# Kernel optimization log

Hardware: AMD Instinct MI355X
Metric: run time of the kernel (lower is better)

## Reference

```python
import jax, jax.numpy as jnp
import numpy as np

HIDDEN = 1024
ATTN = 512


def setup_inputs() -> dict:
    key = jax.random.key(0)
    ks = jax.random.split(key, 7)
    B, S = 8, 2048
    inputs = jax.random.normal(ks[0], (B, S, HIDDEN), dtype=jnp.float32)
    s = 1.0 / np.sqrt(HIDDEN)
    Wq = jax.random.uniform(ks[1], (HIDDEN, ATTN), jnp.float32, -s, s)
    bq = jax.random.uniform(ks[2], (ATTN,), jnp.float32, -s, s)
    Wk = jax.random.uniform(ks[3], (HIDDEN, ATTN), jnp.float32, -s, s)
    bk = jax.random.uniform(ks[4], (ATTN,), jnp.float32, -s, s)
    Wv = jax.random.uniform(ks[5], (HIDDEN, ATTN), jnp.float32, -s, s)
    bv = jax.random.uniform(ks[6], (ATTN,), jnp.float32, -s, s)
    return {"inputs": inputs, "Wq": Wq, "bq": bq, "Wk": Wk, "bk": bk, "Wv": Wv, "bv": bv}


def reference(inputs, Wq, bq, Wk, bk, Wv, bv):
    # tanh-gated Q/K/V projections
    q = jnp.tanh(inputs @ Wq + bq)        # [B, S, A]
    k = jnp.tanh(inputs @ Wk + bk)        # [B, S, A]
    v = jnp.tanh(inputs @ Wv + bv)        # [B, S, A]
    scores = jnp.einsum('bqa,bka->bqk', q, k) / jnp.sqrt(jnp.float32(ATTN))
    probs = jax.nn.softmax(scores, axis=-1)   # [B, S, S]
    context = jnp.einsum('bqk,bka->bqa', probs, v)
    return jnp.tanh(context), probs
```

## Files before the change

kernel.cpp:

```cpp
#include <hip/hip_runtime.h>
#include <hip/hip_fp16.h>
#include <cstdint>

#define HIDDEN 1024
#define ATTN   512
#define NB     8
#define SEQ    2048
#define MROWS  (NB*SEQ)

typedef _Float16 f16x8 __attribute__((ext_vector_type(8)));
typedef _Float16 f16x4 __attribute__((ext_vector_type(4)));
typedef float    f32x4 __attribute__((ext_vector_type(4)));


__device__ __forceinline__ float tanh_fast(float x){
  float e = __expf(2.0f*x);
  return 1.0f - 2.0f/(e + 1.0f);
}

__device__ __forceinline__ void gload16(const void* g, void* l){
  __builtin_amdgcn_global_load_lds((const __attribute__((address_space(1))) void*)g,
                                   (__attribute__((address_space(3))) void*)l, 16, 0, 0);
}

__global__ __launch_bounds__(256) void k_cast_x(const float* __restrict__ x, __half* __restrict__ xh){
  size_t i = (size_t)blockIdx.x*256 + threadIdx.x;
  const float4* src = reinterpret_cast<const float4*>(x) + i*2;
  float4 a = src[0], b = src[1];
  f16x8 h;
  h[0]=(_Float16)a.x; h[1]=(_Float16)a.y; h[2]=(_Float16)a.z; h[3]=(_Float16)a.w;
  h[4]=(_Float16)b.x; h[5]=(_Float16)b.y; h[6]=(_Float16)b.z; h[7]=(_Float16)b.w;
  reinterpret_cast<f16x8*>(xh)[i] = h;
}

__global__ __launch_bounds__(256) void k_transpose_w(const float* __restrict__ Wq, const float* __restrict__ Wk,
                                                     const float* __restrict__ Wv, __half* __restrict__ whT){
  __shared__ float lds[32][33];
  int which = blockIdx.y;
  const float* W = which==0 ? Wq : (which==1 ? Wk : Wv);
  int tr = blockIdx.x >> 4;
  int tc = blockIdx.x & 15;
  int t = threadIdx.x;
  {
    int r = t >> 3, c4 = (t & 7)*4;
    float4 v = *reinterpret_cast<const float4*>(W + (size_t)(tr*32 + r)*ATTN + tc*32 + c4);
    lds[r][c4+0]=v.x; lds[r][c4+1]=v.y; lds[r][c4+2]=v.z; lds[r][c4+3]=v.w;
  }
  __syncthreads();
  {
    int n = t >> 3, k4 = (t & 7)*4;
    ushort4 u;
    u.x = __half_as_ushort(__float2half(lds[k4+0][n]));
    u.y = __half_as_ushort(__float2half(lds[k4+1][n]));
    u.z = __half_as_ushort(__float2half(lds[k4+2][n]));
    u.w = __half_as_ushort(__float2half(lds[k4+3][n]));
    *reinterpret_cast<ushort4*>(whT + (size_t)which*ATTN*HIDDEN + (size_t)(tc*32 + n)*HIDDEN + tr*32 + k4) = u;
  }
}

__global__ __launch_bounds__(256,3) void k_proj(const __half* __restrict__ xh, const __half* __restrict__ whT,
                                                const float* __restrict__ bq, const float* __restrict__ bk,
                                                const float* __restrict__ bv,
                                                __half* __restrict__ qh, __half* __restrict__ kh, __half* __restrict__ vT){
  __shared__ __align__(16) _Float16 lA[128*64];
  __shared__ __align__(16) _Float16 lB[128*64];
  int nt = blockIdx.x;
  int m0 = blockIdx.y * 128;
  int which = nt >> 2;
  int ncol0 = (nt & 3) * 128;
  int t = threadIdx.x;
  int w = t >> 6, lane = t & 63;
  int lrow = lane & 15, lk = lane >> 4;
  int wm = w >> 1, wn = w & 1;

  int rr = lane >> 3;
  int ss = (lane & 7) ^ rr;
  const __half* Abase = xh + (size_t)(m0 + w*32 + rr)*HIDDEN + ss*8;
  const __half* Bbase = whT + (size_t)which*ATTN*HIDDEN + (size_t)(ncol0 + w*32 + rr)*HIDDEN + ss*8;
  _Float16* lAw = &lA[(w*32)*64];
  _Float16* lBw = &lB[(w*32)*64];

  f32x4 acc[4][4];
  #pragma unroll
  for (int i=0;i<4;i++)
    #pragma unroll
    for (int j=0;j<4;j++) acc[i][j] = f32x4{0.f,0.f,0.f,0.f};

  for (int k0 = 0; k0 < HIDDEN; k0 += 64){
    __syncthreads();
    #pragma unroll
    for (int c=0; c<4; c++){
      gload16(Abase + (size_t)c*8*HIDDEN + k0, &lAw[c*8*64]);
      gload16(Bbase + (size_t)c*8*HIDDEN + k0, &lBw[c*8*64]);
    }
    __syncthreads();
    #pragma unroll
    for (int u=0; u<2; u++){
      f16x8 af[4], bf[4];
      #pragma unroll
      for (int fm=0; fm<4; fm++){
        int row = wm*64 + fm*16 + lrow;
        af[fm] = *(const f16x8*)&lA[row*64 + (((u*4 + lk) ^ (row & 7))*8)];
      }
      #pragma unroll
      for (int fn=0; fn<4; fn++){
        int row = wn*64 + fn*16 + lrow;
        bf[fn] = *(const f16x8*)&lB[row*64 + (((u*4 + lk) ^ (row & 7))*8)];
      }
      #pragma unroll
      for (int fm=0; fm<4; fm++)
        #pragma unroll
        for (int fn=0; fn<4; fn++)
          acc[fm][fn] = __builtin_amdgcn_mfma_f32_16x16x32_f16(af[fm], bf[fn], acc[fm][fn], 0,0,0);
    }
  }

  const float* bias = which==0 ? bq : (which==1 ? bk : bv);
  if (which < 2){
    __half* dst = which==0 ? qh : kh;
    int rt_base = (m0 >> 4) + wm*4;
    int at_base = (ncol0 >> 5) + wn*2;
    #pragma unroll
    for (int fn=0; fn<4; fn++){
      int col = ncol0 + wn*64 + fn*16 + lrow;
      float bb = bias[col];
      int at = at_base + (fn >> 1);
      int asub = (fn & 1)*16 + lrow;
      #pragma unroll
      for (int fm=0; fm<4; fm++){
        size_t tbase = (size_t)(rt_base + fm)*8192 + (size_t)at*512 + asub;
        #pragma unroll
        for (int mi=0; mi<4; mi++)
          dst[tbase + (lk*4 + mi)*32] = __float2half(tanh_fast(acc[fm][fn][mi] + bb));
      }
    }
  } else {
    __half* vb = vT + (size_t)(m0 >> 11)*ATTN*SEQ;
    int jb0 = (m0 & 2047) + wm*64;
    int at0 = (ncol0 >> 4) + wn*4;
    #pragma unroll
    for (int fn=0; fn<4; fn++){
      int col = ncol0 + wn*64 + fn*16 + lrow;
      float bb = bias[col];
      #pragma unroll
      for (int fm=0; fm<4; fm++){
        int jb = jb0 + fm*16;
        f16x4 h;
        #pragma unroll
        for (int mi=0; mi<4; mi++) h[mi] = (_Float16)tanh_fast(acc[fm][fn][mi] + bb);
        *(f16x4*)(vb + (size_t)(at0 + fn)*32768 + (size_t)(jb >> 5)*512 + lrow*32 + (jb & 16) + lk*4) = h;
      }
    }
  }
}

__global__ __launch_bounds__(512,2) void k_scoresE(const __half* __restrict__ qh, const __half* __restrict__ kh,
                                                   __half* __restrict__ p16){
  __shared__ __align__(16) _Float16 qlds[4*16*512];
  __shared__ __align__(16) _Float16 khlds[32*512];
  int bid = blockIdx.x;
  int b  = bid & 7;
  int i0 = (bid >> 3) * 64;
  int t = threadIdx.x;
  int w = t >> 6, lane = t & 63;
  int lrow = lane & 15, lk = lane >> 4;

  const __half* qsrc = qh + (size_t)((b*SEQ + i0) >> 4)*8192;
  const __half* ksrc = kh + (size_t)b*SEQ*ATTN;
  __half* pb = p16 + (size_t)b*SEQ*SEQ;

  #pragma unroll
  for (int r=0; r<8; r++){
    int chunk = r*8 + w;
    gload16(qsrc + (size_t)chunk*512 + lane*8, &qlds[chunk*512]);
  }

  const float scale = 0.044194173824159216f;
  for (int ko = 0; ko < 4; ko++){
    f32x4 acc[4][4];
    #pragma unroll
    for (int i=0;i<4;i++)
      #pragma unroll
      for (int j=0;j<4;j++) acc[i][j] = f32x4{0.f,0.f,0.f,0.f};

    for (int it = 0; it < 16; it++){
      __syncthreads();
      #pragma unroll
      for (int j=0; j<4; j++){
        int c = w*4 + j;
        gload16(ksrc + (size_t)(ko*32 + c)*8192 + it*512 + lane*8, &khlds[c*512]);
      }
      __syncthreads();
      f16x8 kf[4], qf[4];
      #pragma unroll
      for (int j=0;j<4;j++) kf[j] = *(const f16x8*)&khlds[(w*4+j)*512 + lrow*32 + lk*8];
      #pragma unroll
      for (int j=0;j<4;j++) qf[j] = *(const f16x8*)&qlds[(j*16 + it)*512 + lrow*32 + lk*8];
      #pragma unroll
      for (int fn=0; fn<4; fn++)
        #pragma unroll
        for (int qi=0; qi<4; qi++)
          acc[qi][fn] = __builtin_amdgcn_mfma_f32_16x16x32_f16(kf[fn], qf[qi], acc[qi][fn], 0,0,0);
    }

    #pragma unroll
    for (int qi=0; qi<4; qi++){
      size_t tq = (size_t)((i0 >> 4) + qi)*32768;
      #pragma unroll
      for (int fn=0; fn<4; fn++){
        f16x4 h;
        #pragma unroll
        for (int mi=0; mi<4; mi++) h[mi] = (_Float16)__expf(acc[qi][fn][mi]*scale);
        *(f16x4*)&pb[tq + (size_t)(ko*16 + w*2 + (fn>>1))*512 + lrow*32 + (fn&1)*16 + lk*4] = h;
      }
    }
  }
}

__global__ __launch_bounds__(1024,4) void k_scores(const __half* __restrict__ qh, const __half* __restrict__ kh,
                                                   float* __restrict__ probs){
  __shared__ float red[16][32];
  int bid = blockIdx.x;
  int b  = bid & 7;
  int i0 = (bid >> 3) * 32;
  int t = threadIdx.x;
  int w = t >> 6, lane = t & 63;
  int lrow = lane & 15, lk = lane >> 4;
  int loff = lrow*32 + lk*8;

  const __half* kbase = kh + (size_t)((b*SEQ + w*128) >> 4)*8192 + loff;
  const __half* qbase = qh + (size_t)((b*SEQ + i0) >> 4)*8192 + loff;

  f32x4 acc[2][8];
  #pragma unroll
  for (int i=0;i<2;i++)
    #pragma unroll
    for (int j=0;j<8;j++) acc[i][j] = f32x4{0.f,0.f,0.f,0.f};

  for (int it = 0; it < 16; it++){
    f16x8 aq0 = *(const f16x8*)(qbase + it*512);
    f16x8 aq1 = *(const f16x8*)(qbase + 8192 + it*512);
    #pragma unroll
    for (int fn=0; fn<8; fn++){
      f16x8 kf = *(const f16x8*)(kbase + (size_t)fn*8192 + it*512);
      acc[0][fn] = __builtin_amdgcn_mfma_f32_16x16x32_f16(kf, aq0, acc[0][fn], 0,0,0);
      acc[1][fn] = __builtin_amdgcn_mfma_f32_16x16x32_f16(kf, aq1, acc[1][fn], 0,0,0);
    }
  }

  const float scale = 0.044194173824159216f;
  float sm[2];
  #pragma unroll
  for (int nf=0;nf<2;nf++){
    float s = 0.f;
    #pragma unroll
    for (int fn=0;fn<8;fn++)
      #pragma unroll
      for (int mi=0;mi<4;mi++){
        float e = __expf(acc[nf][fn][mi] * scale);
        acc[nf][fn][mi] = e;
        s += e;
      }
    s += __shfl_xor(s, 16);
    s += __shfl_xor(s, 32);
    sm[nf] = s;
  }
  if (lane < 16){ red[w][lane] = sm[0]; red[w][16 + lane] = sm[1]; }
  __syncthreads();
  float inv[2];
  #pragma unroll
  for (int nf=0;nf<2;nf++){
    float tot = 0.f;
    #pragma unroll
    for (int ww=0; ww<16; ww++) tot += red[ww][nf*16 + lrow];
    inv[nf] = 1.0f / tot;
  }
  #pragma unroll
  for (int nf=0;nf<2;nf++){
    f32x4 iv = {inv[nf], inv[nf], inv[nf], inv[nf]};
    #pragma unroll
    for (int fn=0;fn<8;fn++){
      f32x4 v = acc[nf][fn] * iv;
      size_t rowoff = (size_t)(i0 + nf*16 + lrow)*SEQ + w*128 + lk*4;
      *(f32x4*)(probs + (size_t)b*SEQ*SEQ + rowoff + fn*16) = v;
    }
  }
}

__global__ __launch_bounds__(512,4) void k_pv_p16(const __half* __restrict__ p16, const __half* __restrict__ vT,
                                                  float* __restrict__ probs, float* __restrict__ out0){
  __shared__ float partial[8][64];
  __shared__ float rsum[64];
  int bid = blockIdx.x;
  int b  = bid & 7;
  int i0 = (bid >> 3) * 64;
  int t = threadIdx.x;
  int w = t >> 6, lane = t & 63;
  int lrow = lane & 15, lk = lane >> 4;
  int loff = lrow*32 + lk*8;

  const __half* pbase = p16 + (size_t)b*SEQ*SEQ + (size_t)(i0 >> 4)*32768 + loff;
  const __half* vbase = vT + (size_t)b*ATTN*SEQ + (size_t)(w*4)*32768 + loff;

  f32x4 acc[4][4];
  #pragma unroll
  for (int i=0;i<4;i++)
    #pragma unroll
    for (int j=0;j<4;j++) acc[i][j] = f32x4{0.f,0.f,0.f,0.f};
  float esum[4] = {0.f,0.f,0.f,0.f};

  for (int kt = 0; kt < 64; kt++){
    f16x8 pa[4];
    #pragma unroll
    for (int nf=0; nf<4; nf++)
      pa[nf] = *(const f16x8*)(pbase + (size_t)nf*32768 + kt*512);
    if ((kt >> 3) == w){
      #pragma unroll
      for (int nf=0; nf<4; nf++){
        float s = 0.f;
        #pragma unroll
        for (int j=0; j<8; j++) s += (float)pa[nf][j];
        esum[nf] += s;
      }
    }
    #pragma unroll
    for (int cf=0; cf<4; cf++){
      f16x8 bv8 = *(const f16x8*)(vbase + (size_t)cf*32768 + kt*512);
      #pragma unroll
      for (int nf=0; nf<4; nf++)
        acc[nf][cf] = __builtin_amdgcn_mfma_f32_16x16x32_f16(pa[nf], bv8, acc[nf][cf], 0,0,0);
    }
  }

  #pragma unroll
  for (int nf=0; nf<4; nf++){
    esum[nf] += __shfl_xor(esum[nf], 16);
    esum[nf] += __shfl_xor(esum[nf], 32);
  }
  if (lane < 16){
    #pragma unroll
    for (int nf=0; nf<4; nf++) partial[w][nf*16 + lane] = esum[nf];
  }
  __syncthreads();
  if (t < 64){
    float s = 0.f;
    #pragma unroll
    for (int ww=0; ww<8; ww++) s += partial[ww][t];
    rsum[t] = s;
  }
  __syncthreads();

  float* dst = out0 + ((size_t)b*SEQ + i0)*ATTN + w*64;
  #pragma unroll
  for (int nf=0; nf<4; nf++)
    #pragma unroll
    for (int mi=0; mi<4; mi++){
      float iv = 1.0f / rsum[nf*16 + lk*4 + mi];
      #pragma unroll
      for (int cf=0; cf<4; cf++)
        __builtin_nontemporal_store(tanh_fast(acc[nf][cf][mi]*iv),
                                    dst + (size_t)(nf*16 + lk*4 + mi)*ATTN + cf*16 + lrow);
    }

  float* prow = probs + ((size_t)b*SEQ + i0 + lrow)*SEQ + lk*8;
  #pragma unroll
  for (int nf=0; nf<4; nf++){
    float iv = 1.0f / rsum[nf*16 + lrow];
    #pragma unroll
    for (int k2=0; k2<8; k2++){
      int kt = w*8 + k2;
      f16x8 pa = *(const f16x8*)(pbase + (size_t)nf*32768 + kt*512);
      f32x4 lo = {(float)pa[0]*iv, (float)pa[1]*iv, (float)pa[2]*iv, (float)pa[3]*iv};
      f32x4 hi = {(float)pa[4]*iv, (float)pa[5]*iv, (float)pa[6]*iv, (float)pa[7]*iv};
      float* pr = prow + (size_t)nf*16*SEQ + kt*32;
      __builtin_nontemporal_store(lo, (f32x4*)(pr));
      __builtin_nontemporal_store(hi, (f32x4*)(pr + 4));
    }
  }
}

__global__ __launch_bounds__(512,4) void k_pv(const float* __restrict__ probs, const __half* __restrict__ vT,
                                              float* __restrict__ out0){
  int bid = blockIdx.x;
  int b  = bid & 7;
  int i0 = (bid >> 3) * 32;
  int t = threadIdx.x;
  int w = t >> 6, lane = t & 63;
  int lrow = lane & 15, lk = lane >> 4;
  int loff = lrow*32 + lk*8;

  const float* pbase = probs + ((size_t)b*SEQ + i0 + lrow)*SEQ + lk*8;
  const __half* vbase = vT + (size_t)b*ATTN*SEQ + (size_t)(w*4)*32768 + loff;

  f32x4 acc[2][4];
  #pragma unroll
  for (int i=0;i<2;i++)
    #pragma unroll
    for (int j=0;j<4;j++) acc[i][j] = f32x4{0.f,0.f,0.f,0.f};

  for (int kt = 0; kt < 64; kt++){
    int k0 = kt*32;
    f16x8 af[2];
    #pragma unroll
    for (int nf=0; nf<2; nf++){
      const float* pr = pbase + (size_t)nf*16*SEQ + k0;
      float4 a = *(const float4*)(pr);
      float4 c = *(const float4*)(pr + 4);
      f16x8 h;
      h[0]=(_Float16)a.x; h[1]=(_Float16)a.y; h[2]=(_Float16)a.z; h[3]=(_Float16)a.w;
      h[4]=(_Float16)c.x; h[5]=(_Float16)c.y; h[6]=(_Float16)c.z; h[7]=(_Float16)c.w;
      af[nf] = h;
    }
    #pragma unroll
    for (int cf=0; cf<4; cf++){
      f16x8 bv8 = *(const f16x8*)(vbase + (size_t)cf*32768 + kt*512);
      acc[0][cf] = __builtin_amdgcn_mfma_f32_16x16x32_f16(af[0], bv8, acc[0][cf], 0,0,0);
      acc[1][cf] = __builtin_amdgcn_mfma_f32_16x16x32_f16(af[1], bv8, acc[1][cf], 0,0,0);
    }
  }

  float* dst = out0 + ((size_t)b*SEQ + i0)*ATTN + w*64;
  #pragma unroll
  for (int nf=0; nf<2; nf++)
    #pragma unroll
    for (int cf=0; cf<4; cf++)
      #pragma unroll
      for (int mi=0; mi<4; mi++)
        dst[(size_t)(nf*16 + lk*4 + mi)*ATTN + cf*16 + lrow] = tanh_fast(acc[nf][cf][mi]);
}

extern "C" void kernel_launch(void* const* d_in, const int* in_sizes, int n_in,
                              void* d_out, int out_size, void* d_ws, size_t ws_size,
                              hipStream_t stream){
  const float* x  = (const float*)d_in[0];
  const float* Wq = (const float*)d_in[1];
  const float* bq = (const float*)d_in[2];
  const float* Wk = (const float*)d_in[3];
  const float* bk = (const float*)d_in[4];
  const float* Wv = (const float*)d_in[5];
  const float* bv = (const float*)d_in[6];

  float* out0 = (float*)d_out;
  float* out1 = out0 + (size_t)NB*SEQ*ATTN;

  const size_t SZ = 16777216;
  char* ws = (char*)d_ws;

  if (ws_size >= 5*SZ){
    __half* vT  = (__half*)ws;
    __half* p16 = (__half*)(ws + SZ);
    __half* xh  = (__half*)out1;
    __half* whT = (__half*)((char*)out1 + 2*SZ);
    __half* qh  = (__half*)((char*)out1 + 2*SZ + 3145728);
    __half* kh  = (__half*)((char*)out1 + 3*SZ + 3145728);
    k_cast_x     <<<8192,        256, 0, stream>>>(x, xh);
    k_transpose_w<<<dim3(512,3), 256, 0, stream>>>(Wq, Wk, Wv, whT);
    k_proj       <<<dim3(12,128),256, 0, stream>>>(xh, whT, bq, bk, bv, qh, kh, vT);
    k_scoresE    <<<256,         512, 0, stream>>>(qh, kh, p16);
    k_pv_p16     <<<256,         512, 0, stream>>>(p16, vT, out1, out0);
  } else if (ws_size >= 3*SZ){
    __half* vT = (__half*)ws;
    __half* qh = (__half*)(ws + SZ);
    __half* kh = (__half*)(ws + 2*SZ);
    __half* xh  = (__half*)out1;
    __half* whT = (__half*)((char*)out1 + 2*SZ);
    k_cast_x     <<<8192,        256, 0, stream>>>(x, xh);
    k_transpose_w<<<dim3(512,3), 256, 0, stream>>>(Wq, Wk, Wv, whT);
    k_proj       <<<dim3(12,128),256, 0, stream>>>(xh, whT, bq, bk, bv, qh, kh, vT);
    k_scores     <<<512,        1024, 0, stream>>>(qh, kh, out1);
    k_pv         <<<512,         512, 0, stream>>>(out1, vT, out0);
  } else {
    __half* vT = (__half*)ws;
    __half* qh = (__half*)out0;
    __half* kh = (__half*)out0 + (size_t)MROWS*ATTN;
    __half* xh  = (__half*)out1;
    __half* whT = (__half*)((char*)out1 + 2*SZ);
    k_cast_x     <<<8192,        256, 0, stream>>>(x, xh);
    k_transpose_w<<<dim3(512,3), 256, 0, stream>>>(Wq, Wk, Wv, whT);
    k_proj       <<<dim3(12,128),256, 0, stream>>>(xh, whT, bq, bk, bv, qh, kh, vT);
    k_scores     <<<512,        1024, 0, stream>>>(qh, kh, out1);
    k_pv         <<<512,         512, 0, stream>>>(out1, vT, out0);
  }
}
```

Before: 282.2 us.

## Split probs expansion and row sums into separate kernel; double K tile per sync

Moves the fp16-to-fp32 probability expansion and the softmax row-sum computation out of the P·V kernel into a new k_expand kernel. That kernel stages a 16-row tile in LDS, reduces the row sums, writes them to workspace and streams out the normalized fp32 probs. The P·V kernel now only does MFMA work plus a normalized tanh epilogue, reading the precomputed sums. The scores kernel also loads two K tiles per barrier pair, halving its syncs at the cost of double the K staging LDS. The risks are an extra launch, rereading p16, and the new path now needing slightly more workspace than before.

```diff
diff --git a/kernel.cpp b/kernel.cpp
--- a/kernel.cpp
+++ b/kernel.cpp
@@ -157,7 +157,7 @@
 __global__ __launch_bounds__(512,2) void k_scoresE(const __half* __restrict__ qh, const __half* __restrict__ kh,
                                                    __half* __restrict__ p16){
   __shared__ __align__(16) _Float16 qlds[4*16*512];
-  __shared__ __align__(16) _Float16 khlds[32*512];
+  __shared__ __align__(16) _Float16 khlds[64*512];
   int bid = blockIdx.x;
   int b  = bid & 7;
   int i0 = (bid >> 3) * 64;
@@ -183,24 +183,28 @@
       #pragma unroll
       for (int j=0;j<4;j++) acc[i][j] = f32x4{0.f,0.f,0.f,0.f};
 
-    for (int it = 0; it < 16; it++){
+    for (int it = 0; it < 16; it += 2){
       __syncthreads();
       #pragma unroll
       for (int j=0; j<4; j++){
         int c = w*4 + j;
-        gload16(ksrc + (size_t)(ko*32 + c)*8192 + it*512 + lane*8, &khlds[c*512]);
+        gload16(ksrc + (size_t)(ko*32 + c)*8192 + it*512 + lane*8,       &khlds[c*512]);
+        gload16(ksrc + (size_t)(ko*32 + c)*8192 + (it+1)*512 + lane*8,   &khlds[(32 + c)*512]);
       }
       __syncthreads();
-      f16x8 kf[4], qf[4];
-      #pragma unroll
-      for (int j=0;j<4;j++) kf[j] = *(const f16x8*)&khlds[(w*4+j)*512 + lrow*32 + lk*8];
-      #pragma unroll
-      for (int j=0;j<4;j++) qf[j] = *(const f16x8*)&qlds[(j*16 + it)*512 + lrow*32 + lk*8];
-      #pragma unroll
-      for (int fn=0; fn<4; fn++)
-        #pragma unroll
-        for (int qi=0; qi<4; qi++)
-          acc[qi][fn] = __builtin_amdgcn_mfma_f32_16x16x32_f16(kf[fn], qf[qi], acc[qi][fn], 0,0,0);
+      #pragma unroll
+      for (int half=0; half<2; half++){
+        f16x8 kf[4], qf[4];
+        #pragma unroll
+        for (int j=0;j<4;j++) kf[j] = *(const f16x8*)&khlds[(half*32 + w*4+j)*512 + lrow*32 + lk*8];
+        #pragma unroll
+        for (int j=0;j<4;j++) qf[j] = *(const f16x8*)&qlds[(j*16 + it + half)*512 + lrow*32 + lk*8];
+        #pragma unroll
+        for (int fn=0; fn<4; fn++)
+          #pragma unroll
+          for (int qi=0; qi<4; qi++)
+            acc[qi][fn] = __builtin_amdgcn_mfma_f32_16x16x32_f16(kf[fn], qf[qi], acc[qi][fn], 0,0,0);
+      }
     }
 
     #pragma unroll
@@ -213,6 +217,63 @@
         for (int mi=0; mi<4; mi++) h[mi] = (_Float16)__expf(acc[qi][fn][mi]*scale);
         *(f16x4*)&pb[tq + (size_t)(ko*16 + w*2 + (fn>>1))*512 + lrow*32 + (fn&1)*16 + lk*4] = h;
       }
+    }
+  }
+}
+
+__global__ __launch_bounds__(256,4) void k_expand(const __half* __restrict__ p16,
+                                                  float* __restrict__ probs, float* __restrict__ rsumg){
+  __shared__ __align__(16) _Float16 lds[16*2048];
+  __shared__ float partial[16][16];
+  __shared__ float rs[16];
+  int bid = blockIdx.x;
+  int b  = bid & 7;
+  int tq = bid >> 3;
+  int t = threadIdx.x;
+  int w = t >> 6, lane = t & 63;
+
+  const __half* src = p16 + (size_t)b*SEQ*SEQ + (size_t)tq*32768;
+  #pragma unroll
+  for (int i=0; i<16; i++){
+    int chunk = i*4 + w;
+    gload16(src + (size_t)chunk*512 + lane*8, &lds[chunk*512]);
+  }
+  __syncthreads();
+
+  {
+    int r = t & 15, seg = t >> 4;
+    float s = 0.f;
+    #pragma unroll
+    for (int c8=0; c8<16; c8++){
+      int c = seg*128 + c8*8;
+      f16x8 v = *(const f16x8*)&lds[(c >> 5)*512 + r*32 + (c & 31)];
+      #pragma unroll
+      for (int j=0;j<8;j++) s += (float)v[j];
+    }
+    partial[seg][r] = s;
+  }
+  __syncthreads();
+  if (t < 16){
+    float s = 0.f;
+    #pragma unroll
+    for (int seg=0; seg<16; seg++) s += partial[seg][t];
+    rs[t] = s;
+    rsumg[(size_t)b*SEQ + tq*16 + t] = s;
+  }
+  __syncthreads();
+
+  float* pbase = probs + ((size_t)b*SEQ + tq*16)*SEQ;
+  #pragma unroll
+  for (int rr=0; rr<4; rr++){
+    int r = rr*4 + w;
+    float iv = 1.0f / rs[r];
+    float* prow = pbase + (size_t)r*SEQ;
+    #pragma unroll
+    for (int ki=0; ki<8; ki++){
+      int c = ki*256 + lane*4;
+      f16x4 v = *(const f16x4*)&lds[(c >> 5)*512 + r*32 + (c & 31)];
+      f32x4 o = {(float)v[0]*iv, (float)v[1]*iv, (float)v[2]*iv, (float)v[3]*iv};
+      __builtin_nontemporal_store(o, (f32x4*)(prow + c));
     }
   }
 }
@@ -288,9 +349,7 @@
 }
 
 __global__ __launch_bounds__(512,4) void k_pv_p16(const __half* __restrict__ p16, const __half* __restrict__ vT,
-                                                  float* __restrict__ probs, float* __restrict__ out0){
-  __shared__ float partial[8][64];
-  __shared__ float rsum[64];
+                                                  const float* __restrict__ rsumg, float* __restrict__ out0){
   int bid = blockIdx.x;
   int b  = bid & 7;
   int i0 = (bid >> 3) * 64;
@@ -307,22 +366,12 @@
   for (int i=0;i<4;i++)
     #pragma unroll
     for (int j=0;j<4;j++) acc[i][j] = f32x4{0.f,0.f,0.f,0.f};
-  float esum[4] = {0.f,0.f,0.f,0.f};
 
   for (int kt = 0; kt < 64; kt++){
     f16x8 pa[4];
     #pragma unroll
     for (int nf=0; nf<4; nf++)
       pa[nf] = *(const f16x8*)(pbase + (size_t)nf*32768 + kt*512);
-    if ((kt >> 3) == w){
-      #pragma unroll
-      for (int nf=0; nf<4; nf++){
-        float s = 0.f;
-        #pragma unroll
-        for (int j=0; j<8; j++) s += (float)pa[nf][j];
-        esum[nf] += s;
-      }
-    }
     #pragma unroll
     for (int cf=0; cf<4; cf++){
       f16x8 bv8 = *(const f16x8*)(vbase + (size_t)cf*32768 + kt*512);
@@ -332,49 +381,17 @@
     }
   }
 
+  float* dst = out0 + ((size_t)b*SEQ + i0)*ATTN + w*64;
   #pragma unroll
   for (int nf=0; nf<4; nf++){
-    esum[nf] += __shfl_xor(esum[nf], 16);
-    esum[nf] += __shfl_xor(esum[nf], 32);
-  }
-  if (lane < 16){
-    #pragma unroll
-    for (int nf=0; nf<4; nf++) partial[w][nf*16 + lane] = esum[nf];
-  }
-  __syncthreads();
-  if (t < 64){
-    float s = 0.f;
-    #pragma unroll
-    for (int ww=0; ww<8; ww++) s += partial[ww][t];
-    rsum[t] = s;
-  }
-  __syncthreads();
-
-  float* dst = out0 + ((size_t)b*SEQ + i0)*ATTN + w*64;
-  #pragma unroll
-  for (int nf=0; nf<4; nf++)
+    f32x4 rs4 = *(const f32x4*)&rsumg[(size_t)b*SEQ + i0 + nf*16 + lk*4];
     #pragma unroll
     for (int mi=0; mi<4; mi++){
-      float iv = 1.0f / rsum[nf*16 + lk*4 + mi];
+      float iv = 1.0f / rs4[mi];
       #pragma unroll
       for (int cf=0; cf<4; cf++)
         __builtin_nontemporal_store(tanh_fast(acc[nf][cf][mi]*iv),
                                     dst + (size_t)(nf*16 + lk*4 + mi)*ATTN + cf*16 + lrow);
-    }
-
-  float* prow = probs + ((size_t)b*SEQ + i0 + lrow)*SEQ + lk*8;
-  #pragma unroll
-  for (int nf=0; nf<4; nf++){
-    float iv = 1.0f / rsum[nf*16 + lrow];
-    #pragma unroll
-    for (int k2=0; k2<8; k2++){
-      int kt = w*8 + k2;
-      f16x8 pa = *(const f16x8*)(pbase + (size_t)nf*32768 + kt*512);
-      f32x4 lo = {(float)pa[0]*iv, (float)pa[1]*iv, (float)pa[2]*iv, (float)pa[3]*iv};
-      f32x4 hi = {(float)pa[4]*iv, (float)pa[5]*iv, (float)pa[6]*iv, (float)pa[7]*iv};
-      float* pr = prow + (size_t)nf*16*SEQ + kt*32;
-      __builtin_nontemporal_store(lo, (f32x4*)(pr));
-      __builtin_nontemporal_store(hi, (f32x4*)(pr + 4));
     }
   }
 }
@@ -446,9 +463,10 @@
   const size_t SZ = 16777216;
   char* ws = (char*)d_ws;
 
-  if (ws_size >= 5*SZ){
-    __half* vT  = (__half*)ws;
-    __half* p16 = (__half*)(ws + SZ);
+  if (ws_size >= 5*SZ + 65536){
+    __half* vT    = (__half*)ws;
+    __half* p16   = (__half*)(ws + SZ);
+    float*  rsumg = (float*)(ws + 5*SZ);
     __half* xh  = (__half*)out1;
     __half* whT = (__half*)((char*)out1 + 2*SZ);
     __half* qh  = (__half*)((char*)out1 + 2*SZ + 3145728);
@@ -457,7 +475,8 @@
     k_transpose_w<<<dim3(512,3), 256, 0, stream>>>(Wq, Wk, Wv, whT);
     k_proj       <<<dim3(12,128),256, 0, stream>>>(xh, whT, bq, bk, bv, qh, kh, vT);
     k_scoresE    <<<256,         512, 0, stream>>>(qh, kh, p16);
-    k_pv_p16     <<<256,         512, 0, stream>>>(p16, vT, out1, out0);
+    k_expand     <<<1024,        256, 0, stream>>>(p16, out1, rsumg);
+    k_pv_p16     <<<256,         512, 0, stream>>>(p16, vT, rsumg, out0);
   } else if (ws_size >= 3*SZ){
     __half* vT = (__half*)ws;
     __half* qh = (__half*)(ws + SZ);
```

After: 266.2 us (median of 2 runs). 5.7% less time.
